# Kernel optimization log

Hardware: AMD Instinct MI355X
Metric: run time of the kernel (lower is better)

## Reference

```python
import jax, jax.numpy as jnp
import numpy as np

B, S, F = 32, 4096, 256
G, N = 2, 128           # num_groups, num_entries_per_group
D = F // G              # group_dim = 128
E = 256                 # embed_dim


def setup_inputs() -> dict:
    key = jax.random.key(0)
    ks = jax.random.split(key, 6)
    return {
        "features": jax.random.normal(ks[0], (B, S, F), jnp.float32),
        "gumbel": jax.random.gumbel(ks[1], (B, S, G, N), jnp.float32),
        "W_logits": jax.random.normal(ks[2], (G, D, N), jnp.float32) * (1.0 / np.sqrt(D)),
        "b_logits": jnp.zeros((G, N), jnp.float32),
        "codebooks": jax.random.normal(ks[3], (G, N, D), jnp.float32) * 0.02,
        "W_out": jax.random.normal(ks[4], (F, E), jnp.float32) * (1.0 / np.sqrt(F)),
        "b_out": jnp.zeros((E,), jnp.float32),
    }


def reference(features, gumbel, W_logits, b_logits, codebooks, W_out, b_out):
    b, s, f = features.shape
    grouped = features.reshape(b, s, G, D)                       # [B,S,G,D]
    logits = jnp.einsum("bsgd,gdn->bsgn", grouped, W_logits) + b_logits
    noisy = logits + gumbel                                      # training=True
    soft = jax.nn.softmax(noisy, axis=-1)                        # [B,S,G,N]
    hard_idx = jnp.argmax(noisy, axis=-1)                        # [B,S,G] int
    hard = jax.nn.one_hot(hard_idx, N, dtype=soft.dtype)
    st = jax.lax.stop_gradient(hard - soft) + soft               # straight-through
    quantized = jnp.einsum("bsgn,gnd->bsgd", st, codebooks)      # [B,S,G,D]
    quantized = quantized.reshape(b, s, G * D)                   # [B,S,F]
    out = quantized @ W_out + b_out                              # [B,S,E]
    indices = hard_idx.astype(jnp.int32)                         # [B,S,G]
    return out, indices
```

## Files before the change

### kernel.cpp

```cpp
#include <hip/hip_runtime.h>

#define T_TOTAL (32 * 4096)
#define FDIM 256
#define NG 2
#define NN 128
#define DDIM 128
#define EDIM 256

#define TAU 0.004f
#define CAP 16384

typedef __attribute__((ext_vector_type(4))) float f32x4;
typedef __attribute__((ext_vector_type(8))) short short8;

__global__ __launch_bounds__(256) void prep_kernel(
    const float* __restrict__ codebooks,
    const float* __restrict__ W_out,
    const float* __restrict__ Wl,
    float* __restrict__ CO,
    short* __restrict__ BT,
    int* __restrict__ flag_count)
{
    const int gn  = blockIdx.x;
    const int g   = gn >> 7;
    const int tid = threadIdx.x;
    __shared__ float cb[DDIM];
    if (tid < DDIM) cb[tid] = codebooks[gn * DDIM + tid];
    if (tid >= 128) {
        const int k = tid - 128;
        const int n = gn & 127;
        const float x = Wl[((size_t)g * DDIM + k) * NN + n];
        const unsigned u = __float_as_uint(x);
        const float hi = __uint_as_float(u & 0xffff0000u);
        const unsigned u2 = __float_as_uint(x - hi);
        BT[(size_t)g * 16384 + n * 128 + k] = (short)(u >> 16);
        BT[32768 + (size_t)g * 16384 + n * 128 + k] = (short)(u2 >> 16);
    }
    if (gn == 0 && tid == 0) *flag_count = 0;
    __syncthreads();
    float acc = 0.f;
    const float* wcol = W_out + (g * DDIM) * EDIM + tid;
#pragma unroll 4
    for (int d = 0; d < DDIM; ++d) acc += cb[d] * wcol[d * EDIM];
    CO[gn * EDIM + tid] = acc;
}

__global__ __launch_bounds__(512) void pq_v15_kernel(
    const float* __restrict__ features,
    const float* __restrict__ gumbel,
    const short* __restrict__ BT,
    const float* __restrict__ bl,
    float* __restrict__ idx_f,
    int* __restrict__ flag_count,
    int* __restrict__ flag_list)
{
    __shared__ short8 Flds[2048];
    __shared__ float pm1s[8][64];
    __shared__ float pm2s[8][64];
    __shared__ int   pi1s[8][64];

    const int tid  = threadIdx.x;
    const int g    = blockIdx.x & 1;
    const int span = blockIdx.x >> 1;
    const int w    = tid >> 6;
    const int l    = tid & 63;
    const int q    = l & 15;
    const int h    = l >> 4;
    const int n0   = w * 16;
    const int tb0  = span * 256;

    const short* bt1 = BT + (size_t)g * 16384 + (n0 + q) * 128 + h * 8;
    short8 A1[4], A2[4];
#pragma unroll
    for (int ks = 0; ks < 4; ++ks) {
        A1[ks] = *reinterpret_cast<const short8*>(bt1 + ks * 32);
        A2[ks] = *reinterpret_cast<const short8*>(bt1 + 32768 + ks * 32);
    }
    const f32x4 bv = *reinterpret_cast<const f32x4*>(bl + g * NN + n0 + h * 4);

    const int stok = tid >> 3;
    const int skc  = tid & 7;
    const int swz  = stok & 7;

    const float* fstage = features + (size_t)(tb0 + stok) * FDIM + g * DDIM + skc * 16;
    const float* gq     = gumbel + ((size_t)(tb0 + q) * NG + g) * NN + n0 + h * 4;

    f32x4 F[4];
    f32x4 G[4];

#pragma unroll
    for (int j = 0; j < 4; ++j)
        F[j] = *reinterpret_cast<const f32x4*>(fstage + j * 4);

#pragma unroll
    for (int st = 0; st < 4; ++st) {
        short8 SH0, SH1, SL0, SL1;
#pragma unroll
        for (int e = 0; e < 4; ++e) {
            unsigned u; float hi;
            u = __float_as_uint(F[0][e]); hi = __uint_as_float(u & 0xffff0000u);
            SH0[e]     = (short)(u >> 16); SL0[e]     = (short)(__float_as_uint(F[0][e] - hi) >> 16);
            u = __float_as_uint(F[1][e]); hi = __uint_as_float(u & 0xffff0000u);
            SH0[4 + e] = (short)(u >> 16); SL0[4 + e] = (short)(__float_as_uint(F[1][e] - hi) >> 16);
            u = __float_as_uint(F[2][e]); hi = __uint_as_float(u & 0xffff0000u);
            SH1[e]     = (short)(u >> 16); SL1[e]     = (short)(__float_as_uint(F[2][e] - hi) >> 16);
            u = __float_as_uint(F[3][e]); hi = __uint_as_float(u & 0xffff0000u);
            SH1[4 + e] = (short)(u >> 16); SL1[4 + e] = (short)(__float_as_uint(F[3][e] - hi) >> 16);
        }

        __syncthreads();

        {
            short8* rowHi = Flds + stok * 16;
            short8* rowLo = Flds + 1024 + stok * 16;
            rowHi[(2 * skc)     ^ swz] = SH0;
            rowHi[(2 * skc + 1) ^ swz] = SH1;
            rowLo[(2 * skc)     ^ swz] = SL0;
            rowLo[(2 * skc + 1) ^ swz] = SL1;
        }

        if (st > 0 && tid < 64) {
            float c1 = pm1s[0][tid], c2 = pm2s[0][tid];
            int   ci = pi1s[0][tid];
#pragma unroll
            for (int p = 1; p < 8; ++p) {
                const float a1 = pm1s[p][tid];
                const float a2 = pm2s[p][tid];
                const int   ai = pi1s[p][tid];
                if (a1 > c1)      { c2 = fmaxf(c1, a2); c1 = a1; ci = ai; }
                else if (a1 < c1) { c2 = fmaxf(c2, a1); }
                else              { c2 = c1; ci = min(ci, ai); }
            }
            const int t = tb0 + (st - 1) * 64 + tid;
            idx_f[(size_t)t * NG + g] = (float)ci;
            if (c1 - c2 < TAU) {
                const int p = atomicAdd(flag_count, 1);
                if (p < CAP) flag_list[p] = t * NG + g;
            }
        }

        __syncthreads();

        if (st < 3) {
            const float* fp = fstage + (size_t)(st + 1) * 64 * FDIM;
#pragma unroll
            for (int j = 0; j < 4; ++j)
                F[j] = *reinterpret_cast<const f32x4*>(fp + j * 4);
        }
#pragma unroll
        for (int s = 0; s < 4; ++s)
            G[s] = *reinterpret_cast<const f32x4*>(
                gq + (size_t)(st * 64 + s * 16) * NG * NN);

#pragma unroll
        for (int s = 0; s < 4; ++s) {
            const int rbase = (s * 16 + q) * 16;
            f32x4 acc = (f32x4){0.f, 0.f, 0.f, 0.f};
#pragma unroll
            for (int ks = 0; ks < 4; ++ks) {
                const int ci0 = (ks * 4 + h) ^ (q & 7);
                const short8 B1 = Flds[rbase + ci0];
                const short8 B2 = Flds[1024 + rbase + ci0];
                acc = __builtin_amdgcn_mfma_f32_16x16x32_bf16(A1[ks], B1, acc, 0, 0, 0);
                acc = __builtin_amdgcn_mfma_f32_16x16x32_bf16(A2[ks], B1, acc, 0, 0, 0);
                acc = __builtin_amdgcn_mfma_f32_16x16x32_bf16(A1[ks], B2, acc, 0, 0, 0);
            }

            float m1 = -3.4e38f, m2 = -3.4e38f;
            int   i1 = 0;
#pragma unroll
            for (int r = 0; r < 4; ++r) {
                const float vv = acc[r] + bv[r] + G[s][r];
                const int   n  = n0 + h * 4 + r;
                if (vv > m1) { m2 = m1; m1 = vv; i1 = n; }
                else         { m2 = fmaxf(m2, vv); }
            }
#pragma unroll
            for (int off = 16; off < 64; off <<= 1) {
                const float om1 = __shfl_xor(m1, off);
                const int   oi1 = __shfl_xor(i1, off);
                const float om2 = __shfl_xor(m2, off);
                if (om1 > m1)      { m2 = fmaxf(m1, om2); m1 = om1; i1 = oi1; }
                else if (om1 < m1) { m2 = fmaxf(m2, om1); }
                else               { m2 = m1; i1 = min(i1, oi1); }
            }
            if (h == 0) {
                pm1s[w][s * 16 + q] = m1;
                pm2s[w][s * 16 + q] = m2;
                pi1s[w][s * 16 + q] = i1;
            }
        }
    }

    __syncthreads();
    if (tid < 64) {
        float c1 = pm1s[0][tid], c2 = pm2s[0][tid];
        int   ci = pi1s[0][tid];
#pragma unroll
        for (int p = 1; p < 8; ++p) {
            const float a1 = pm1s[p][tid];
            const float a2 = pm2s[p][tid];
            const int   ai = pi1s[p][tid];
            if (a1 > c1)      { c2 = fmaxf(c1, a2); c1 = a1; ci = ai; }
            else if (a1 < c1) { c2 = fmaxf(c2, a1); }
            else              { c2 = c1; ci = min(ci, ai); }
        }
        const int t = tb0 + 3 * 64 + tid;
        idx_f[(size_t)t * NG + g] = (float)ci;
        if (c1 - c2 < TAU) {
            const int p = atomicAdd(flag_count, 1);
            if (p < CAP) flag_list[p] = t * NG + g;
        }
    }
}

__global__ __launch_bounds__(128) void fixup_kernel(
    const float* __restrict__ features,
    const float* __restrict__ gumbel,
    const float* __restrict__ Wl,
    const float* __restrict__ bl,
    float* __restrict__ idx_f,
    const int* __restrict__ flag_count,
    const int* __restrict__ flag_list)
{
    __shared__ float sm[2];
    __shared__ int   si[2];
    int total = *flag_count;
    if (total > CAP) total = CAP;
    const int n = threadIdx.x;

    for (int e = blockIdx.x; e < total; e += gridDim.x) {
        const int code = flag_list[e];
        const int t = code >> 1, g = code & 1;
        const float* fpr = features + (size_t)t * FDIM + g * DDIM;
        const float* wp  = Wl + (size_t)g * DDIM * NN + n;
        float dot = 0.f;
#pragma unroll 8
        for (int k = 0; k < DDIM; ++k) dot = fmaf(fpr[k], wp[(size_t)k * NN], dot);
        const float v = (dot + bl[g * NN + n]) + gumbel[((size_t)t * NG + g) * NN + n];

        float m = v; int bi = n;
#pragma unroll
        for (int off = 1; off < 64; off <<= 1) {
            const float om = __shfl_xor(m, off);
            const int   ob = __shfl_xor(bi, off);
            if (om > m || (om == m && ob < bi)) { m = om; bi = ob; }
        }
        if ((n & 63) == 0) { sm[n >> 6] = m; si[n >> 6] = bi; }
        __syncthreads();
        if (n == 0) {
            const float mA = sm[0], mB = sm[1];
            const int bA = si[0], bB = si[1];
            const int best = (mB > mA || (mB == mA && bB < bA)) ? bB : bA;
            idx_f[code] = (float)best;
        }
        __syncthreads();
    }
}

__global__ __launch_bounds__(256) void out_kernel(
    const float* __restrict__ CO,
    const float* __restrict__ b_out,
    const float* __restrict__ idx_f,
    float* __restrict__ out)
{
    const int tid = threadIdx.x;
    const int e4  = tid & 63;
    const int ts  = tid >> 6;
    const int tbase = blockIdx.x * 16;
    const float4 b = *reinterpret_cast<const float4*>(b_out + e4 * 4);

#pragma unroll
    for (int it = 0; it < 4; ++it) {
        const int t  = tbase + it * 4 + ts;
        const int i0 = (int)idx_f[t * NG + 0];
        const int i1 = (int)idx_f[t * NG + 1];
        const float4 c0 = *reinterpret_cast<const float4*>(CO + (size_t)i0 * EDIM + e4 * 4);
        const float4 c1 = *reinterpret_cast<const float4*>(CO + (size_t)(NN + i1) * EDIM + e4 * 4);
        float4 o;
        o.x = c0.x + c1.x + b.x;
        o.y = c0.y + c1.y + b.y;
        o.z = c0.z + c1.z + b.z;
        o.w = c0.w + c1.w + b.w;
        *reinterpret_cast<float4*>(out + (size_t)t * EDIM + e4 * 4) = o;
    }
}

extern "C" void kernel_launch(void* const* d_in, const int* in_sizes, int n_in,
                              void* d_out, int out_size, void* d_ws, size_t ws_size,
                              hipStream_t stream) {
    const float* features  = (const float*)d_in[0];
    const float* gumbel    = (const float*)d_in[1];
    const float* Wl        = (const float*)d_in[2];
    const float* bl        = (const float*)d_in[3];
    const float* codebooks = (const float*)d_in[4];
    const float* W_out     = (const float*)d_in[5];
    const float* b_out     = (const float*)d_in[6];

    float* out   = (float*)d_out;
    float* idx_f = out + (size_t)T_TOTAL * EDIM;

    char* ws = (char*)d_ws;
    float* CO         = (float*)ws;
    short* BT         = (short*)(ws + 262144);
    int*   flag_count = (int*)(ws + 262144 + 131072);
    int*   flag_list  = (int*)(ws + 393216 + 256);

    prep_kernel<<<NG * NN, 256, 0, stream>>>(codebooks, W_out, Wl, CO, BT, flag_count);
    pq_v15_kernel<<<1024, 512, 0, stream>>>(
        features, gumbel, BT, bl, idx_f, flag_count, flag_list);
    fixup_kernel<<<1024, 128, 0, stream>>>(
        features, gumbel, Wl, bl, idx_f, flag_count, flag_list);
    out_kernel<<<T_TOTAL / 16, 256, 0, stream>>>(CO, b_out, idx_f, out);
}
```

Before: 132.2 us.

## Stage gumbel tiles through LDS with coalesced prefetch and inline-asm global loads

Gumbel noise is now loaded with the same coalesced per-token pattern as features (each thread loads 16 contiguous floats of one token row) and staged into a padded LDS buffer. Each wave then reads its logit slice from LDS, replacing the earlier strided per-lane global loads. Features and gumbel for the next stage are prefetched with inline-asm global_load_dwordx4 and an explicit vmcnt(0) wait plus a sched_barrier, so the loads overlap the MFMA work. The cost is about 33KB of extra LDS, which may cut occupancy, and hand-placed waits that limit what the compiler can schedule.

```diff
diff --git a/kernel.cpp b/kernel.cpp
--- a/kernel.cpp
+++ b/kernel.cpp
@@ -9,6 +9,8 @@
 
 #define TAU 0.004f
 #define CAP 16384
+
+#define GROW 132
 
 typedef __attribute__((ext_vector_type(4))) float f32x4;
 typedef __attribute__((ext_vector_type(8))) short short8;
@@ -45,7 +47,7 @@
     CO[gn * EDIM + tid] = acc;
 }
 
-__global__ __launch_bounds__(512) void pq_v15_kernel(
+__global__ __launch_bounds__(512) void pq_v17_kernel(
     const float* __restrict__ features,
     const float* __restrict__ gumbel,
     const short* __restrict__ BT,
@@ -55,6 +57,7 @@
     int* __restrict__ flag_list)
 {
     __shared__ short8 Flds[2048];
+    __shared__ __align__(16) float Glds[64 * GROW];
     __shared__ float pm1s[8][64];
     __shared__ float pm2s[8][64];
     __shared__ int   pi1s[8][64];
@@ -83,29 +86,37 @@
     const int swz  = stok & 7;
 
     const float* fstage = features + (size_t)(tb0 + stok) * FDIM + g * DDIM + skc * 16;
-    const float* gq     = gumbel + ((size_t)(tb0 + q) * NG + g) * NN + n0 + h * 4;
-
-    f32x4 F[4];
-    f32x4 G[4];
-
-#pragma unroll
-    for (int j = 0; j < 4; ++j)
-        F[j] = *reinterpret_cast<const f32x4*>(fstage + j * 4);
+    const float* gstage = gumbel + ((size_t)(tb0 + stok) * NG + g) * NN + skc * 16;
+
+    f32x4 Fr[4], Gr[4];
+
+#define GLOAD(dst, ptr) \
+    asm volatile("global_load_dwordx4 %0, %1, off" : "=v"(dst) : "v"(ptr))
+#define VWAIT0() do { \
+    asm volatile("s_waitcnt vmcnt(0)" ::: "memory"); \
+    __builtin_amdgcn_sched_barrier(0); } while (0)
+
+    GLOAD(Fr[0], fstage);     GLOAD(Fr[1], fstage + 4);
+    GLOAD(Fr[2], fstage + 8); GLOAD(Fr[3], fstage + 12);
+    GLOAD(Gr[0], gstage);     GLOAD(Gr[1], gstage + 4);
+    GLOAD(Gr[2], gstage + 8); GLOAD(Gr[3], gstage + 12);
 
 #pragma unroll
     for (int st = 0; st < 4; ++st) {
+        VWAIT0();
+
         short8 SH0, SH1, SL0, SL1;
 #pragma unroll
         for (int e = 0; e < 4; ++e) {
             unsigned u; float hi;
-            u = __float_as_uint(F[0][e]); hi = __uint_as_float(u & 0xffff0000u);
-            SH0[e]     = (short)(u >> 16); SL0[e]     = (short)(__float_as_uint(F[0][e] - hi) >> 16);
-            u = __float_as_uint(F[1][e]); hi = __uint_as_float(u & 0xffff0000u);
-            SH0[4 + e] = (short)(u >> 16); SL0[4 + e] = (short)(__float_as_uint(F[1][e] - hi) >> 16);
-            u = __float_as_uint(F[2][e]); hi = __uint_as_float(u & 0xffff0000u);
-            SH1[e]     = (short)(u >> 16); SL1[e]     = (short)(__float_as_uint(F[2][e] - hi) >> 16);
-            u = __float_as_uint(F[3][e]); hi = __uint_as_float(u & 0xffff0000u);
-            SH1[4 + e] = (short)(u >> 16); SL1[4 + e] = (short)(__float_as_uint(F[3][e] - hi) >> 16);
+            u = __float_as_uint(Fr[0][e]); hi = __uint_as_float(u & 0xffff0000u);
+            SH0[e]     = (short)(u >> 16); SL0[e]     = (short)(__float_as_uint(Fr[0][e] - hi) >> 16);
+            u = __float_as_uint(Fr[1][e]); hi = __uint_as_float(u & 0xffff0000u);
+            SH0[4 + e] = (short)(u >> 16); SL0[4 + e] = (short)(__float_as_uint(Fr[1][e] - hi) >> 16);
+            u = __float_as_uint(Fr[2][e]); hi = __uint_as_float(u & 0xffff0000u);
+            SH1[e]     = (short)(u >> 16); SL1[e]     = (short)(__float_as_uint(Fr[2][e] - hi) >> 16);
+            u = __float_as_uint(Fr[3][e]); hi = __uint_as_float(u & 0xffff0000u);
+            SH1[4 + e] = (short)(u >> 16); SL1[4 + e] = (short)(__float_as_uint(Fr[3][e] - hi) >> 16);
         }
 
         __syncthreads();
@@ -117,6 +128,11 @@
             rowHi[(2 * skc + 1) ^ swz] = SH1;
             rowLo[(2 * skc)     ^ swz] = SL0;
             rowLo[(2 * skc + 1) ^ swz] = SL1;
+            float* grp = Glds + stok * GROW + skc * 16;
+            *reinterpret_cast<f32x4*>(grp)      = Gr[0];
+            *reinterpret_cast<f32x4*>(grp + 4)  = Gr[1];
+            *reinterpret_cast<f32x4*>(grp + 8)  = Gr[2];
+            *reinterpret_cast<f32x4*>(grp + 12) = Gr[3];
         }
 
         if (st > 0 && tid < 64) {
@@ -143,14 +159,12 @@
 
         if (st < 3) {
             const float* fp = fstage + (size_t)(st + 1) * 64 * FDIM;
-#pragma unroll
-            for (int j = 0; j < 4; ++j)
-                F[j] = *reinterpret_cast<const f32x4*>(fp + j * 4);
-        }
-#pragma unroll
-        for (int s = 0; s < 4; ++s)
-            G[s] = *reinterpret_cast<const f32x4*>(
-                gq + (size_t)(st * 64 + s * 16) * NG * NN);
+            const float* gp = gstage + (size_t)(st + 1) * 64 * NG * NN;
+            GLOAD(Fr[0], fp);     GLOAD(Fr[1], fp + 4);
+            GLOAD(Fr[2], fp + 8); GLOAD(Fr[3], fp + 12);
+            GLOAD(Gr[0], gp);     GLOAD(Gr[1], gp + 4);
+            GLOAD(Gr[2], gp + 8); GLOAD(Gr[3], gp + 12);
+        }
 
 #pragma unroll
         for (int s = 0; s < 4; ++s) {
@@ -166,11 +180,14 @@
                 acc = __builtin_amdgcn_mfma_f32_16x16x32_bf16(A1[ks], B2, acc, 0, 0, 0);
             }
 
+            const f32x4 gvv = *reinterpret_cast<const f32x4*>(
+                &Glds[(s * 16 + q) * GROW + n0 + h * 4]);
+
             float m1 = -3.4e38f, m2 = -3.4e38f;
             int   i1 = 0;
 #pragma unroll
             for (int r = 0; r < 4; ++r) {
-                const float vv = acc[r] + bv[r] + G[s][r];
+                const float vv = acc[r] + bv[r] + gvv[r];
                 const int   n  = n0 + h * 4 + r;
                 if (vv > m1) { m2 = m1; m1 = vv; i1 = n; }
                 else         { m2 = fmaxf(m2, vv); }
@@ -191,6 +208,8 @@
             }
         }
     }
+#undef GLOAD
+#undef VWAIT0
 
     __syncthreads();
     if (tid < 64) {
@@ -307,7 +326,7 @@
     int*   flag_list  = (int*)(ws + 393216 + 256);
 
     prep_kernel<<<NG * NN, 256, 0, stream>>>(codebooks, W_out, Wl, CO, BT, flag_count);
-    pq_v15_kernel<<<1024, 512, 0, stream>>>(
+    pq_v17_kernel<<<1024, 512, 0, stream>>>(
         features, gumbel, BT, bl, idx_f, flag_count, flag_list);
     fixup_kernel<<<1024, 128, 0, stream>>>(
         features, gumbel, Wl, bl, idx_f, flag_count, flag_list);
```

Result: slower. 140.3 us (+6.1%).
